# Optimization experiments

Measured on AMD Instinct MI355X. Metric: run time of the kernel, lower is better.

Reference implementation:

```python
import jax, jax.numpy as jnp
import numpy as np

EPS = 1e-6
TTT_BASE_LR = 1.0
NUM_HEADS = 16


def _ln_fused_l2_bwd(x, l2_target, gamma, beta, eps=EPS):
    # Gradient of ||LN(x)*gamma+beta - target||^2/2 wrt x (fused LN + L2 bwd).
    mu = x.mean(axis=-1, keepdims=True)
    var = ((x - mu) ** 2).mean(axis=-1, keepdims=True)
    std = jnp.sqrt(var + eps)
    x_hat = (x - mu) / std
    grad_x_hat = (gamma * x_hat + beta - l2_target) * gamma
    z = (grad_x_hat
         - grad_x_hat.mean(axis=-1, keepdims=True)
         - x_hat * (grad_x_hat * x_hat).mean(axis=-1, keepdims=True)) / std
    return z


def _ln_fwd(x, gamma, beta, eps=EPS):
    mu = x.mean(axis=-1, keepdims=True)
    var = ((x - mu) ** 2).mean(axis=-1, keepdims=True)
    x_hat = (x - mu) / jnp.sqrt(var + eps)
    return gamma * x_hat + beta


def setup_inputs() -> dict:
    key = jax.random.key(0)
    ks = jax.random.split(key, 6)
    B, L, C, H = 2, 2048, 1024, NUM_HEADS
    D = C // H
    return {
        "hidden_states": jax.random.normal(ks[0], (B, L, C), jnp.float32),
        "Wq": jax.random.normal(ks[1], (C, C), jnp.float32) * 0.02,
        "Wk": jax.random.normal(ks[2], (C, C), jnp.float32) * 0.02,
        "Wv": jax.random.normal(ks[3], (C, C), jnp.float32) * 0.02,
        "W1": jax.random.normal(ks[4], (H, D, D), jnp.float32) * 0.02,
        "b1": jnp.zeros((H, 1, D), jnp.float32),
        "ttt_norm_weight": jnp.ones((H, D), jnp.float32),
        "ttt_norm_bias": jnp.zeros((H, D), jnp.float32),
        "lr_weight": jax.random.normal(ks[5], (H, C, 1), jnp.float32) * 0.02,
        "lr_bias": jnp.zeros((H, 1), jnp.float32),
    }


def reference(hidden_states, Wq, Wk, Wv, W1, b1,
              ttt_norm_weight, ttt_norm_bias, lr_weight, lr_bias):
    B, L, C = hidden_states.shape
    H = NUM_HEADS
    D = C // H

    def proj(W):  # nn.Linear(no bias): x @ W^T, then split heads -> [B,H,L,D]
        return (hidden_states @ W.T).reshape(B, L, H, D).transpose(0, 2, 1, 3)

    XQ, XK, XV = proj(Wq), proj(Wk), proj(Wv)

    # adaptive per-token learning rate eta: [B,H,L,1]
    ttt_lr = jnp.einsum("blc,hci->bhli", hidden_states, lr_weight)
    ttt_lr = jax.nn.sigmoid(ttt_lr + lr_bias.reshape(1, H, 1, 1))
    eta = TTT_BASE_LR * ttt_lr / D

    # inner-loop forward with initial fast weights W1,b1
    Z1 = jnp.einsum("bhld,hdf->bhlf", XK, W1) + b1[None]  # [B,H,L,D]
    recon_target = XV - XK

    gamma = ttt_norm_weight.reshape(1, H, 1, D)
    beta = ttt_norm_bias.reshape(1, H, 1, D)
    grad_l_wrt_Z1 = _ln_fused_l2_bwd(Z1, recon_target, gamma, beta)

    # dual form update (batch-parallel, no state carry)
    eg = eta * grad_l_wrt_Z1                               # [B,H,L,D]
    Attn1 = jnp.einsum("bhld,bhmd->bhlm", XQ, XK)          # [B,H,L,L]
    b1_bar = b1[None] - eg.sum(axis=2, keepdims=True)      # [B,H,1,D]
    Z1_bar = (jnp.einsum("bhld,hdf->bhlf", XQ, W1)
              - jnp.einsum("bhlm,bhmd->bhld", Attn1, eg)
              + b1_bar)

    Z1_normalized = _ln_fwd(Z1_bar, gamma, beta)
    return XQ + Z1_normalized  # [B,H,L,D]
```

## Files before the change

### kernel.cpp

```cpp
#include <hip/hip_runtime.h>
#include <math.h>

#define B_ 2
#define L_ 2048
#define C_ 1024
#define H_ 16
#define D_ 64
#define BH_ (B_*H_)
#define M_ (B_*L_)
#define N_ (3*C_)
#define K_ C_
#define EPS_ 1e-6f
#define NCHUNK_ 16
#define LDT_ 136

typedef unsigned short ushort_t;
typedef short short8 __attribute__((ext_vector_type(8)));
typedef float f32x4 __attribute__((ext_vector_type(4)));
typedef unsigned short ushort4_t __attribute__((ext_vector_type(4)));

__device__ __forceinline__ ushort_t f2bf(float f) {
    union { float f; unsigned u; } v; v.f = f;
    unsigned r = v.u + 0x7FFFu + ((v.u >> 16) & 1u);
    return (ushort_t)(r >> 16);
}
__device__ __forceinline__ float bf2f(ushort_t h) {
    union { unsigned u; float f; } v; v.u = ((unsigned)h) << 16;
    return v.f;
}

__device__ __forceinline__ void gload16(const void* g, void* l) {
    __builtin_amdgcn_global_load_lds(
        (const __attribute__((address_space(1))) void*)g,
        (__attribute__((address_space(3))) void*)l, 16, 0, 0);
}

__global__ __launch_bounds__(256) void cast_eta(
    const float* __restrict__ hs, const float* __restrict__ Wq,
    const float* __restrict__ Wk, const float* __restrict__ Wv,
    const float* __restrict__ lrw, const float* __restrict__ lrb,
    ushort_t* __restrict__ hsB, ushort_t* __restrict__ Wcat,
    float* __restrict__ eta) {
    __shared__ float pA[16][257], pB[16][257];
    const int bid = blockIdx.x, t = threadIdx.x;
    if (bid < 2048) {
        const int iA = bid * 2, iB = iA + 1;
        const float* rA = hs + (size_t)iA * C_;
        const float* rB = hs + (size_t)iB * C_;
        f32x4 a = *(const f32x4*)(rA + t * 4);
        f32x4 b = *(const f32x4*)(rB + t * 4);
        ushort4_t oa, ob;
        oa.x = f2bf(a.x); oa.y = f2bf(a.y); oa.z = f2bf(a.z); oa.w = f2bf(a.w);
        ob.x = f2bf(b.x); ob.y = f2bf(b.y); ob.z = f2bf(b.z); ob.w = f2bf(b.w);
        *(ushort4_t*)(hsB + (size_t)iA * C_ + t * 4) = oa;
        *(ushort4_t*)(hsB + (size_t)iB * C_ + t * 4) = ob;
        #pragma unroll
        for (int h = 0; h < 16; ++h) {
            f32x4 w = *(const f32x4*)(lrw + (size_t)h * C_ + t * 4);
            pA[h][t] = a.x * w.x + a.y * w.y + a.z * w.z + a.w * w.w;
            pB[h][t] = b.x * w.x + b.y * w.y + b.z * w.z + b.w * w.w;
        }
        __syncthreads();
        const int h = t >> 4, seg = t & 15;
        float sA = 0.f, sB = 0.f;
        #pragma unroll
        for (int j = 0; j < 16; ++j) {
            sA += pA[h][seg * 16 + j];
            sB += pB[h][seg * 16 + j];
        }
        #pragma unroll
        for (int m = 1; m < 16; m <<= 1) {
            sA += __shfl_xor(sA, m, 64);
            sB += __shfl_xor(sB, m, 64);
        }
        if (seg == 0) {
            float bb = lrb[h];
            int bA = iA >> 11, lA = iA & (L_ - 1);
            int bB = iB >> 11, lB = iB & (L_ - 1);
            eta[((size_t)(bA * H_ + h)) * L_ + lA] =
                (1.f / (1.f + expf(-(sA + bb)))) * (1.0f / 64.0f);
            eta[((size_t)(bB * H_ + h)) * L_ + lB] =
                (1.f / (1.f + expf(-(sB + bb)))) * (1.0f / 64.0f);
        }
    } else {
        const int wb = bid - 2048;
        #pragma unroll
        for (int ii = 0; ii < 4; ++ii) {
            int cid = wb * 1024 + ii * 256 + t;
            int m = cid >> 18, r = cid & ((1 << 18) - 1);
            const float* src = (m == 0 ? Wq : (m == 1 ? Wk : Wv));
            f32x4 v = *(const f32x4*)(src + (size_t)r * 4);
            ushort4_t o;
            o.x = f2bf(v.x); o.y = f2bf(v.y); o.z = f2bf(v.z); o.w = f2bf(v.w);
            *(ushort4_t*)(Wcat + (size_t)m * (C_ * C_) + (size_t)r * 4) = o;
        }
    }
}

__global__ __launch_bounds__(256) void gemm_qkv(
    const ushort_t* __restrict__ A, const ushort_t* __restrict__ Bc,
    ushort_t* __restrict__ XQ, ushort_t* __restrict__ XK,
    ushort_t* __restrict__ XV) {
    __shared__ __align__(16) ushort_t Al[128 * 32];
    __shared__ __align__(16) ushort_t Bl[128 * 32];
    const int lid = blockIdx.x + 32 * blockIdx.y;
    const int nid = (lid & 7) * 96 + (lid >> 3);
    const int bm = nid & 31, bn = nid >> 5;
    const int t = threadIdx.x, w = t >> 6, lane = t & 63;
    const int wr = w >> 1, wc = w & 1;
    f32x4 acc[4][4];
    #pragma unroll
    for (int a = 0; a < 4; a++)
        #pragma unroll
        for (int b = 0; b < 4; b++)
            #pragma unroll
            for (int j = 0; j < 4; j++) acc[a][b][j] = 0.f;

    const int ci0 = w * 64 + lane;
    const int xread = ((lane & 15) >> 1) & 3;
    const int uslot = (lane >> 4) ^ xread;

    for (int kt = 0; kt < K_ / 32; ++kt) {
        __syncthreads();
        #pragma unroll
        for (int q = 0; q < 2; ++q) {
            int ci = q * 256 + ci0;
            int r = ci >> 2, kc = ci & 3;
            int kcp = kc ^ ((r >> 1) & 3);
            gload16(A + (size_t)(bm * 128 + r) * K_ + kt * 32 + kcp * 8,
                    &Al[q * 2048 + w * 512]);
            gload16(Bc + (size_t)(bn * 128 + r) * K_ + kt * 32 + kcp * 8,
                    &Bl[q * 2048 + w * 512]);
        }
        __syncthreads();
        short8 af[4], bfv[4];
        #pragma unroll
        for (int mf = 0; mf < 4; ++mf)
            af[mf] = *(const short8*)&Al[(wr * 64 + mf * 16 + (lane & 15)) * 32 + uslot * 8];
        #pragma unroll
        for (int nf = 0; nf < 4; ++nf)
            bfv[nf] = *(const short8*)&Bl[(wc * 64 + nf * 16 + (lane & 15)) * 32 + uslot * 8];
        #pragma unroll
        for (int mf = 0; mf < 4; ++mf)
            #pragma unroll
            for (int nf = 0; nf < 4; ++nf)
                acc[mf][nf] = __builtin_amdgcn_mfma_f32_16x16x32_bf16(
                    af[mf], bfv[nf], acc[mf][nf], 0, 0, 0);
    }

    const int jbase = bn * 128;
    const int mtx = jbase >> 10;
    ushort_t* dst = (mtx == 0) ? XQ : (mtx == 1 ? XK : XV);
    #pragma unroll
    for (int mf = 0; mf < 4; ++mf)
        #pragma unroll
        for (int nf = 0; nf < 4; ++nf)
            #pragma unroll
            for (int rg = 0; rg < 4; ++rg) {
                int i = bm * 128 + wr * 64 + mf * 16 + ((lane >> 4) << 2) + rg;
                int j = (jbase & 1023) + wc * 64 + nf * 16 + (lane & 15);
                int b = i >> 11, l = i & (L_ - 1);
                int h = j >> 6, d = j & 63;
                dst[((size_t)(b * H_ + h) * L_ + l) * D_ + d] = f2bf(acc[mf][nf][rg]);
            }
}

__global__ __launch_bounds__(256) void k2_grad2(
    const ushort_t* __restrict__ XK, const ushort_t* __restrict__ XV,
    const float* __restrict__ W1, const float* __restrict__ b1,
    const float* __restrict__ tw, const float* __restrict__ tb,
    const float* __restrict__ eta, float* __restrict__ Gp,
    float* __restrict__ bsump) {
    __shared__ __align__(16) ushort_t W1t[64 * 64];
    __shared__ __align__(16) ushort_t xkt[64 * LDT_];
    __shared__ __align__(16) ushort_t egl[64 * LDT_];
    __shared__ float b1s[64], gs[64], bes[64];
    __shared__ float sred[4][64];
    const int bh = blockIdx.y, lt = blockIdx.x;
    const int h = bh & (H_ - 1);
    const int t = threadIdx.x, w = t >> 6, lane = t & 63;
    for (int p = t; p < 4096; p += 256) {
        int e = p >> 6, f = p & 63;
        W1t[f * 64 + e] = f2bf(W1[h * 4096 + p]);
    }
    if (t < 64) { b1s[t] = b1[h * 64 + t]; gs[t] = tw[h * 64 + t]; bes[t] = tb[h * 64 + t]; }
    __syncthreads();

    const ushort_t* xk = XK + (size_t)bh * L_ * D_;
    const ushort_t* xv = XV + (size_t)bh * L_ * D_;
    const int l0 = lt * 128 + w * 32;
    const int llw = w * 32;

    f32x4 acc[2][4];
    #pragma unroll
    for (int mf = 0; mf < 2; mf++)
        #pragma unroll
        for (int nf = 0; nf < 4; nf++) {
            float bv = b1s[nf * 16 + (lane & 15)];
            #pragma unroll
            for (int j = 0; j < 4; j++) acc[mf][nf][j] = bv;
        }
    #pragma unroll
    for (int ks = 0; ks < 2; ++ks) {
        short8 af[2], bfv[4];
        const int d0 = ks * 32 + (lane >> 4) * 8;
        #pragma unroll
        for (int mf = 0; mf < 2; mf++) {
            af[mf] = *(const short8*)&xk[(size_t)(l0 + mf * 16 + (lane & 15)) * D_ + d0];
            const int ll = llw + mf * 16 + (lane & 15);
            #pragma unroll
            for (int jj = 0; jj < 8; jj++)
                xkt[(d0 + jj) * LDT_ + ll] = (ushort_t)af[mf][jj];
        }
        #pragma unroll
        for (int nf = 0; nf < 4; nf++)
            bfv[nf] = *(const short8*)&W1t[(nf * 16 + (lane & 15)) * 64 + d0];
        #pragma unroll
        for (int mf = 0; mf < 2; mf++)
            #pragma unroll
            for (int nf = 0; nf < 4; nf++)
                acc[mf][nf] = __builtin_amdgcn_mfma_f32_16x16x32_bf16(
                    af[mf], bfv[nf], acc[mf][nf], 0, 0, 0);
    }

    const float* etap = eta + (size_t)bh * L_;
    float accbs[4] = {0.f, 0.f, 0.f, 0.f};
    #pragma unroll
    for (int mf = 0; mf < 2; ++mf) {
        #pragma unroll
        for (int rg = 0; rg < 4; ++rg) {
            int lrow = l0 + mf * 16 + ((lane >> 4) << 2) + rg;
            int llr  = llw + mf * 16 + ((lane >> 4) << 2) + rg;
            float x[4], xh[4], gh[4];
            #pragma unroll
            for (int nf = 0; nf < 4; nf++) x[nf] = acc[mf][nf][rg];
            float s = x[0] + x[1] + x[2] + x[3];
            s += __shfl_xor(s, 1, 64); s += __shfl_xor(s, 2, 64);
            s += __shfl_xor(s, 4, 64); s += __shfl_xor(s, 8, 64);
            float mu = s * (1.f / 64.f);
            float vs = 0.f;
            #pragma unroll
            for (int nf = 0; nf < 4; nf++) { float dd = x[nf] - mu; vs += dd * dd; }
            vs += __shfl_xor(vs, 1, 64); vs += __shfl_xor(vs, 2, 64);
            vs += __shfl_xor(vs, 4, 64); vs += __shfl_xor(vs, 8, 64);
            float inv = 1.f / sqrtf(vs * (1.f / 64.f) + EPS_);
            float s1 = 0.f, s2 = 0.f;
            #pragma unroll
            for (int nf = 0; nf < 4; nf++) {
                int d = nf * 16 + (lane & 15);
                xh[nf] = (x[nf] - mu) * inv;
                float tgt = bf2f(xv[(size_t)lrow * D_ + d]) - bf2f(xk[(size_t)lrow * D_ + d]);
                float g = gs[d];
                gh[nf] = (g * xh[nf] + bes[d] - tgt) * g;
                s1 += gh[nf]; s2 += gh[nf] * xh[nf];
            }
            s1 += __shfl_xor(s1, 1, 64); s1 += __shfl_xor(s1, 2, 64);
            s1 += __shfl_xor(s1, 4, 64); s1 += __shfl_xor(s1, 8, 64);
            s2 += __shfl_xor(s2, 1, 64); s2 += __shfl_xor(s2, 2, 64);
            s2 += __shfl_xor(s2, 4, 64); s2 += __shfl_xor(s2, 8, 64);
            float m1 = s1 * (1.f / 64.f), m2 = s2 * (1.f / 64.f);
            float el = etap[lrow];
            #pragma unroll
            for (int nf = 0; nf < 4; nf++) {
                int d = nf * 16 + (lane & 15);
                float egv = el * ((gh[nf] - m1 - xh[nf] * m2) * inv);
                accbs[nf] += egv;
                egl[d * LDT_ + llr] = f2bf(egv);
            }
        }
    }
    #pragma unroll
    for (int nf = 0; nf < 4; nf++) {
        accbs[nf] += __shfl_xor(accbs[nf], 16, 64);
        accbs[nf] += __shfl_xor(accbs[nf], 32, 64);
    }
    if (lane < 16)
        #pragma unroll
        for (int nf = 0; nf < 4; nf++) sred[w][nf * 16 + lane] = accbs[nf];
    __syncthreads();

    f32x4 aG[4];
    #pragma unroll
    for (int nf = 0; nf < 4; nf++)
        #pragma unroll
        for (int j = 0; j < 4; j++) aG[nf][j] = 0.f;
    #pragma unroll
    for (int ks = 0; ks < 4; ++ks) {
        const int ko = ks * 32 + (lane >> 4) * 8;
        short8 ae = *(const short8*)&xkt[(w * 16 + (lane & 15)) * LDT_ + ko];
        #pragma unroll
        for (int nf = 0; nf < 4; nf++) {
            short8 be = *(const short8*)&egl[(nf * 16 + (lane & 15)) * LDT_ + ko];
            aG[nf] = __builtin_amdgcn_mfma_f32_16x16x32_bf16(ae, be, aG[nf], 0, 0, 0);
        }
    }
    float* gp = Gp + (size_t)(bh * NCHUNK_ + lt) * 4096;
    #pragma unroll
    for (int nf = 0; nf < 4; nf++)
        #pragma unroll
        for (int rg = 0; rg < 4; rg++) {
            int e = w * 16 + ((lane >> 4) << 2) + rg;
            int d = nf * 16 + (lane & 15);
            gp[e * 64 + d] = aG[nf][rg];
        }
    if (t < 64)
        bsump[(bh * NCHUNK_ + lt) * 64 + t] =
            sred[0][t] + sred[1][t] + sred[2][t] + sred[3][t];
}

__global__ __launch_bounds__(256) void k3_out(
    const ushort_t* __restrict__ XQ, const float* __restrict__ W1,
    const float* __restrict__ Gp, const float* __restrict__ b1,
    const float* __restrict__ bsump, const float* __restrict__ tw,
    const float* __restrict__ tb, float* __restrict__ out) {
    __shared__ __align__(16) ushort_t Wt[64 * 64];
    __shared__ float b1s[64], gs[64], bes[64];
    const int bh = blockIdx.y, lt = blockIdx.x;
    const int h = bh & (H_ - 1);
    const int t = threadIdx.x, w = t >> 6, lane = t & 63;
    for (int p = t; p < 4096; p += 256) {
        int e = p >> 6, f = p & 63;
        float s = W1[h * 4096 + p];
        #pragma unroll
        for (int c = 0; c < NCHUNK_; c++)
            s -= Gp[(size_t)(bh * NCHUNK_ + c) * 4096 + p];
        Wt[f * 64 + e] = f2bf(s);
    }
    if (t < 64) {
        float s = b1[h * 64 + t];
        #pragma unroll
        for (int c = 0; c < NCHUNK_; c++)
            s -= bsump[(bh * NCHUNK_ + c) * 64 + t];
        b1s[t] = s;
        gs[t] = tw[h * 64 + t]; bes[t] = tb[h * 64 + t];
    }
    __syncthreads();

    const ushort_t* xq = XQ + (size_t)bh * L_ * D_;
    const int l0 = lt * 128 + w * 32;
    f32x4 acc[2][4];
    #pragma unroll
    for (int mf = 0; mf < 2; mf++)
        #pragma unroll
        for (int nf = 0; nf < 4; nf++) {
            float bv = b1s[nf * 16 + (lane & 15)];
            #pragma unroll
            for (int j = 0; j < 4; j++) acc[mf][nf][j] = bv;
        }
    #pragma unroll
    for (int ks = 0; ks < 2; ++ks) {
        short8 af[2], bfv[4];
        #pragma unroll
        for (int mf = 0; mf < 2; mf++)
            af[mf] = *(const short8*)&xq[(size_t)(l0 + mf * 16 + (lane & 15)) * D_ + ks * 32 + (lane >> 4) * 8];
        #pragma unroll
        for (int nf = 0; nf < 4; nf++)
            bfv[nf] = *(const short8*)&Wt[(nf * 16 + (lane & 15)) * 64 + ks * 32 + (lane >> 4) * 8];
        #pragma unroll
        for (int mf = 0; mf < 2; mf++)
            #pragma unroll
            for (int nf = 0; nf < 4; nf++)
                acc[mf][nf] = __builtin_amdgcn_mfma_f32_16x16x32_bf16(
                    af[mf], bfv[nf], acc[mf][nf], 0, 0, 0);
    }

    float* outp = out + (size_t)bh * L_ * D_;
    #pragma unroll
    for (int mf = 0; mf < 2; ++mf) {
        #pragma unroll
        for (int rg = 0; rg < 4; ++rg) {
            int lrow = l0 + mf * 16 + ((lane >> 4) << 2) + rg;
            float x[4];
            #pragma unroll
            for (int nf = 0; nf < 4; nf++) x[nf] = acc[mf][nf][rg];
            float s = x[0] + x[1] + x[2] + x[3];
            s += __shfl_xor(s, 1, 64); s += __shfl_xor(s, 2, 64);
            s += __shfl_xor(s, 4, 64); s += __shfl_xor(s, 8, 64);
            float mu = s * (1.f / 64.f);
            float vs = 0.f;
            #pragma unroll
            for (int nf = 0; nf < 4; nf++) { float dd = x[nf] - mu; vs += dd * dd; }
            vs += __shfl_xor(vs, 1, 64); vs += __shfl_xor(vs, 2, 64);
            vs += __shfl_xor(vs, 4, 64); vs += __shfl_xor(vs, 8, 64);
            float inv = 1.f / sqrtf(vs * (1.f / 64.f) + EPS_);
            #pragma unroll
            for (int nf = 0; nf < 4; nf++) {
                int d = nf * 16 + (lane & 15);
                float xh = (x[nf] - mu) * inv;
                float o = gs[d] * xh + bes[d];
                float qv = bf2f(xq[(size_t)lrow * D_ + d]);
                outp[(size_t)lrow * D_ + d] = qv + o;
            }
        }
    }
}

extern "C" void kernel_launch(void* const* d_in, const int* in_sizes, int n_in,
                              void* d_out, int out_size, void* d_ws, size_t ws_size,
                              hipStream_t stream) {
    const float* hs  = (const float*)d_in[0];
    const float* Wq  = (const float*)d_in[1];
    const float* Wk  = (const float*)d_in[2];
    const float* Wv  = (const float*)d_in[3];
    const float* W1  = (const float*)d_in[4];
    const float* b1  = (const float*)d_in[5];
    const float* tw  = (const float*)d_in[6];
    const float* tb  = (const float*)d_in[7];
    const float* lrw = (const float*)d_in[8];
    const float* lrb = (const float*)d_in[9];
    float* out = (float*)d_out;

    char* ws = (char*)d_ws;
    size_t off = 0;
    ushort_t* hsB  = (ushort_t*)(ws + off); off += (size_t)M_ * K_ * 2;
    ushort_t* Wcat = (ushort_t*)(ws + off); off += (size_t)N_ * K_ * 2;
    ushort_t* XQ   = (ushort_t*)(ws + off); off += (size_t)M_ * C_ * 2;
    ushort_t* XK   = (ushort_t*)(ws + off); off += (size_t)M_ * C_ * 2;
    ushort_t* XV   = (ushort_t*)(ws + off); off += (size_t)M_ * C_ * 2;
    float*    eta  = (float*)(ws + off);    off += (size_t)BH_ * L_ * 4;
    float*    Gp    = (float*)hsB;
    float*    bsump = (float*)Wcat;

    cast_eta<<<2048 + 768, 256, 0, stream>>>(hs, Wq, Wk, Wv, lrw, lrb, hsB, Wcat, eta);
    gemm_qkv<<<dim3(M_ / 128, N_ / 128), 256, 0, stream>>>(hsB, Wcat, XQ, XK, XV);
    k2_grad2<<<dim3(L_ / 128, BH_), 256, 0, stream>>>(XK, XV, W1, b1, tw, tb, eta, Gp, bsump);
    k3_out<<<dim3(L_ / 128, BH_), 256, 0, stream>>>(XQ, W1, Gp, b1, bsump, tw, tb, out);
}
```

Measured before the change: 81.93 us.

## Rewrite QKV GEMM with 256x256 tiles and double-buffered LDS prefetch

The QKV projection GEMM is restructured around 256x256 output tiles with 512 threads, a K-step of 64 and two LDS buffers. The next K tile's global-to-LDS loads are interleaved between MFMA phases, with barriers and s_setprio around the compute bursts, so load latency overlaps with matrix math. An XOR swizzle keeps LDS reads conflict-free. The trade-off is the grid: it shrinks to 192 blocks, fewer than the CUs, and the old XCD-aware block remapping is dropped, so some hardware may sit idle. The larger LDS footprint also likely allows only one block per CU.

New measurement: 82.87 us. About the same (+1.1%).

```diff
diff --git a/kernel.cpp b/kernel.cpp
--- a/kernel.cpp
+++ b/kernel.cpp
@@ -97,70 +97,123 @@
     }
 }
 
-__global__ __launch_bounds__(256) void gemm_qkv(
+__global__ __launch_bounds__(512, 2) void gemm_qkv(
     const ushort_t* __restrict__ A, const ushort_t* __restrict__ Bc,
     ushort_t* __restrict__ XQ, ushort_t* __restrict__ XK,
     ushort_t* __restrict__ XV) {
-    __shared__ __align__(16) ushort_t Al[128 * 32];
-    __shared__ __align__(16) ushort_t Bl[128 * 32];
-    const int lid = blockIdx.x + 32 * blockIdx.y;
-    const int nid = (lid & 7) * 96 + (lid >> 3);
-    const int bm = nid & 31, bn = nid >> 5;
-    const int t = threadIdx.x, w = t >> 6, lane = t & 63;
-    const int wr = w >> 1, wc = w & 1;
-    f32x4 acc[4][4];
-    #pragma unroll
-    for (int a = 0; a < 4; a++)
-        #pragma unroll
-        for (int b = 0; b < 4; b++)
-            #pragma unroll
-            for (int j = 0; j < 4; j++) acc[a][b][j] = 0.f;
-
-    const int ci0 = w * 64 + lane;
-    const int xread = ((lane & 15) >> 1) & 3;
-    const int uslot = (lane >> 4) ^ xread;
-
-    for (int kt = 0; kt < K_ / 32; ++kt) {
-        __syncthreads();
-        #pragma unroll
-        for (int q = 0; q < 2; ++q) {
-            int ci = q * 256 + ci0;
-            int r = ci >> 2, kc = ci & 3;
-            int kcp = kc ^ ((r >> 1) & 3);
-            gload16(A + (size_t)(bm * 128 + r) * K_ + kt * 32 + kcp * 8,
-                    &Al[q * 2048 + w * 512]);
-            gload16(Bc + (size_t)(bn * 128 + r) * K_ + kt * 32 + kcp * 8,
-                    &Bl[q * 2048 + w * 512]);
-        }
-        __syncthreads();
-        short8 af[4], bfv[4];
-        #pragma unroll
-        for (int mf = 0; mf < 4; ++mf)
-            af[mf] = *(const short8*)&Al[(wr * 64 + mf * 16 + (lane & 15)) * 32 + uslot * 8];
+    __shared__ __align__(16) ushort_t Al[2][256 * 64];
+    __shared__ __align__(16) ushort_t Bl[2][256 * 64];
+    const int bm = blockIdx.x, bn = blockIdx.y;
+    const int t = threadIdx.x, lane = t & 63, w = t >> 6;
+    const int wm = w >> 2, wn = w & 3;
+    f32x4 acc[8][4];
+    #pragma unroll
+    for (int mf = 0; mf < 8; ++mf)
         #pragma unroll
         for (int nf = 0; nf < 4; ++nf)
-            bfv[nf] = *(const short8*)&Bl[(wc * 64 + nf * 16 + (lane & 15)) * 32 + uslot * 8];
+            #pragma unroll
+            for (int j = 0; j < 4; ++j) acc[mf][nf][j] = 0.f;
+
+#define STAGE_PASS(bi, kt, p) do {                                          \
+        int li_ = (p) * 512 + t; int r_ = li_ >> 3;                         \
+        int us_ = (li_ & 7) ^ (r_ & 7);                                     \
+        gload16(A + (size_t)(bm * 256 + r_) * K_ + (kt) * 64 + us_ * 8,     \
+                &Al[bi][li_ * 8]);                                          \
+        gload16(Bc + (size_t)(bn * 256 + r_) * K_ + (kt) * 64 + us_ * 8,    \
+                &Bl[bi][li_ * 8]);                                          \
+    } while (0)
+
+    const int la15 = lane & 15, la4 = lane >> 4;
+#define RD_A(bi, mf, ks) (*(const short8*)&Al[bi][                          \
+        (wm * 128 + (mf) * 16 + la15) * 64 +                                \
+        ((((ks) * 4 + la4) ^ ((wm * 128 + (mf) * 16 + la15) & 7)) * 8)])
+#define RD_B(bi, nf, ks) (*(const short8*)&Bl[bi][                          \
+        (wn * 64 + (nf) * 16 + la15) * 64 +                                 \
+        ((((ks) * 4 + la4) ^ ((wn * 64 + (nf) * 16 + la15) & 7)) * 8)])
+
+    STAGE_PASS(0, 0, 0); STAGE_PASS(0, 0, 1);
+    STAGE_PASS(0, 0, 2); STAGE_PASS(0, 0, 3);
+    asm volatile("s_waitcnt vmcnt(0)" ::: "memory");
+    __builtin_amdgcn_s_barrier();
+
+    for (int kt = 0; kt < 16; ++kt) {
+        const int c = kt & 1;
+        const bool pf = (kt < 15);
+        short8 bf0[4], bf1[4], afr[4];
+        #pragma unroll
+        for (int nf = 0; nf < 4; ++nf) bf0[nf] = RD_B(c, nf, 0);
+        #pragma unroll
+        for (int mf = 0; mf < 4; ++mf) afr[mf] = RD_A(c, mf, 0);
+        if (pf) { STAGE_PASS(c ^ 1, kt + 1, 0); STAGE_PASS(c ^ 1, kt + 1, 1); }
+        __builtin_amdgcn_s_barrier();
+        __builtin_amdgcn_s_setprio(1);
         #pragma unroll
         for (int mf = 0; mf < 4; ++mf)
             #pragma unroll
             for (int nf = 0; nf < 4; ++nf)
                 acc[mf][nf] = __builtin_amdgcn_mfma_f32_16x16x32_bf16(
-                    af[mf], bfv[nf], acc[mf][nf], 0, 0, 0);
-    }
-
-    const int jbase = bn * 128;
-    const int mtx = jbase >> 10;
+                    afr[mf], bf0[nf], acc[mf][nf], 0, 0, 0);
+        __builtin_amdgcn_s_setprio(0);
+        __builtin_amdgcn_s_barrier();
+        #pragma unroll
+        for (int nf = 0; nf < 4; ++nf) bf1[nf] = RD_B(c, nf, 1);
+        #pragma unroll
+        for (int mf = 0; mf < 4; ++mf) afr[mf] = RD_A(c, mf, 1);
+        if (pf) STAGE_PASS(c ^ 1, kt + 1, 2);
+        __builtin_amdgcn_s_barrier();
+        __builtin_amdgcn_s_setprio(1);
+        #pragma unroll
+        for (int mf = 0; mf < 4; ++mf)
+            #pragma unroll
+            for (int nf = 0; nf < 4; ++nf)
+                acc[mf][nf] = __builtin_amdgcn_mfma_f32_16x16x32_bf16(
+                    afr[mf], bf1[nf], acc[mf][nf], 0, 0, 0);
+        __builtin_amdgcn_s_setprio(0);
+        __builtin_amdgcn_s_barrier();
+        #pragma unroll
+        for (int mf = 0; mf < 4; ++mf) afr[mf] = RD_A(c, mf + 4, 0);
+        if (pf) STAGE_PASS(c ^ 1, kt + 1, 3);
+        __builtin_amdgcn_s_barrier();
+        __builtin_amdgcn_s_setprio(1);
+        #pragma unroll
+        for (int mf = 0; mf < 4; ++mf)
+            #pragma unroll
+            for (int nf = 0; nf < 4; ++nf)
+                acc[mf + 4][nf] = __builtin_amdgcn_mfma_f32_16x16x32_bf16(
+                    afr[mf], bf0[nf], acc[mf + 4][nf], 0, 0, 0);
+        __builtin_amdgcn_s_setprio(0);
+        __builtin_amdgcn_s_barrier();
+        #pragma unroll
+        for (int mf = 0; mf < 4; ++mf) afr[mf] = RD_A(c, mf + 4, 1);
+        __builtin_amdgcn_s_barrier();
+        __builtin_amdgcn_s_setprio(1);
+        #pragma unroll
+        for (int mf = 0; mf < 4; ++mf)
+            #pragma unroll
+            for (int nf = 0; nf < 4; ++nf)
+                acc[mf + 4][nf] = __builtin_amdgcn_mfma_f32_16x16x32_bf16(
+                    afr[mf], bf1[nf], acc[mf + 4][nf], 0, 0, 0);
+        __builtin_amdgcn_s_setprio(0);
+        asm volatile("s_waitcnt vmcnt(0)" ::: "memory");
+        __builtin_amdgcn_s_barrier();
+    }
+#undef STAGE_PASS
+#undef RD_A
+#undef RD_B
+
+    const int mtx = bn >> 2;
     ushort_t* dst = (mtx == 0) ? XQ : (mtx == 1 ? XK : XV);
-    #pragma unroll
-    for (int mf = 0; mf < 4; ++mf)
+    const int jb = (bn & 3) * 256 + wn * 64;
+    #pragma unroll
+    for (int mf = 0; mf < 8; ++mf)
         #pragma unroll
         for (int nf = 0; nf < 4; ++nf)
             #pragma unroll
             for (int rg = 0; rg < 4; ++rg) {
-                int i = bm * 128 + wr * 64 + mf * 16 + ((lane >> 4) << 2) + rg;
-                int j = (jbase & 1023) + wc * 64 + nf * 16 + (lane & 15);
+                int i = bm * 256 + wm * 128 + mf * 16 + la4 * 4 + rg;
+                int jj = jb + nf * 16 + la15;
                 int b = i >> 11, l = i & (L_ - 1);
-                int h = j >> 6, d = j & 63;
+                int h = jj >> 6, d = jj & 63;
                 dst[((size_t)(b * H_ + h) * L_ + l) * D_ + d] = f2bf(acc[mf][nf][rg]);
             }
 }
@@ -422,7 +475,7 @@
     float*    bsump = (float*)Wcat;
 
     cast_eta<<<2048 + 768, 256, 0, stream>>>(hs, Wq, Wk, Wv, lrw, lrb, hsB, Wcat, eta);
-    gemm_qkv<<<dim3(M_ / 128, N_ / 128), 256, 0, stream>>>(hsB, Wcat, XQ, XK, XV);
+    gemm_qkv<<<dim3(M_ / 256, N_ / 256), 512, 0, stream>>>(hsB, Wcat, XQ, XK, XV);
     k2_grad2<<<dim3(L_ / 128, BH_), 256, 0, stream>>>(XK, XV, W1, b1, tw, tb, eta, Gp, bsump);
     k3_out<<<dim3(L_ / 128, BH_), 256, 0, stream>>>(XQ, W1, Gp, b1, bsump, tw, tb, out);
 }
```

## Fold Wv-Wk into weights, stage GEMM epilogue via LDS, drop tile swizzle

Applied to the files above, without the earlier changes.

The weight-cast step now builds the third projection matrix as Wv-Wk, so the GEMM writes the reconstruction target directly and the gradient kernel reads one bf16 tensor instead of two. The GEMM epilogue now stages the accumulator tile in shared memory and writes 16-byte vectors per row, replacing scattered 2-byte stores into the head-major layout. The block-index remapping that grouped tiles for L2 reuse is removed and plain blockIdx order is used. Subtracting the weights in fp32 before rounding to bf16 slightly changes numerics, and the epilogue adds extra barriers and a larger shared-memory footprint.

Result: no change. 80.62 us (-1.6%).

```diff
diff --git a/kernel.cpp b/kernel.cpp
--- a/kernel.cpp
+++ b/kernel.cpp
@@ -88,8 +88,15 @@
         for (int ii = 0; ii < 4; ++ii) {
             int cid = wb * 1024 + ii * 256 + t;
             int m = cid >> 18, r = cid & ((1 << 18) - 1);
-            const float* src = (m == 0 ? Wq : (m == 1 ? Wk : Wv));
-            f32x4 v = *(const f32x4*)(src + (size_t)r * 4);
+            f32x4 v;
+            if (m == 0)      v = *(const f32x4*)(Wq + (size_t)r * 4);
+            else if (m == 1) v = *(const f32x4*)(Wk + (size_t)r * 4);
+            else {
+                f32x4 vv = *(const f32x4*)(Wv + (size_t)r * 4);
+                f32x4 vk = *(const f32x4*)(Wk + (size_t)r * 4);
+                v.x = vv.x - vk.x; v.y = vv.y - vk.y;
+                v.z = vv.z - vk.z; v.w = vv.w - vk.w;
+            }
             ushort4_t o;
             o.x = f2bf(v.x); o.y = f2bf(v.y); o.z = f2bf(v.z); o.w = f2bf(v.w);
             *(ushort4_t*)(Wcat + (size_t)m * (C_ * C_) + (size_t)r * 4) = o;
@@ -100,14 +107,14 @@
 __global__ __launch_bounds__(256) void gemm_qkv(
     const ushort_t* __restrict__ A, const ushort_t* __restrict__ Bc,
     ushort_t* __restrict__ XQ, ushort_t* __restrict__ XK,
-    ushort_t* __restrict__ XV) {
-    __shared__ __align__(16) ushort_t Al[128 * 32];
-    __shared__ __align__(16) ushort_t Bl[128 * 32];
-    const int lid = blockIdx.x + 32 * blockIdx.y;
-    const int nid = (lid & 7) * 96 + (lid >> 3);
-    const int bm = nid & 31, bn = nid >> 5;
+    ushort_t* __restrict__ XT) {
+    __shared__ __align__(16) ushort_t smem[128 * 136];
+    ushort_t* Al = smem;
+    ushort_t* Bl = smem + 4096;
+    const int bm = blockIdx.x, bn = blockIdx.y;
     const int t = threadIdx.x, w = t >> 6, lane = t & 63;
     const int wr = w >> 1, wc = w & 1;
+    const int la15 = lane & 15, la4 = lane >> 4;
     f32x4 acc[4][4];
     #pragma unroll
     for (int a = 0; a < 4; a++)
@@ -117,8 +124,8 @@
             for (int j = 0; j < 4; j++) acc[a][b][j] = 0.f;
 
     const int ci0 = w * 64 + lane;
-    const int xread = ((lane & 15) >> 1) & 3;
-    const int uslot = (lane >> 4) ^ xread;
+    const int xread = (la15 >> 1) & 3;
+    const int uslot = la4 ^ xread;
 
     for (int kt = 0; kt < K_ / 32; ++kt) {
         __syncthreads();
@@ -136,10 +143,10 @@
         short8 af[4], bfv[4];
         #pragma unroll
         for (int mf = 0; mf < 4; ++mf)
-            af[mf] = *(const short8*)&Al[(wr * 64 + mf * 16 + (lane & 15)) * 32 + uslot * 8];
+            af[mf] = *(const short8*)&Al[(wr * 64 + mf * 16 + la15) * 32 + uslot * 8];
         #pragma unroll
         for (int nf = 0; nf < 4; ++nf)
-            bfv[nf] = *(const short8*)&Bl[(wc * 64 + nf * 16 + (lane & 15)) * 32 + uslot * 8];
+            bfv[nf] = *(const short8*)&Bl[(wc * 64 + nf * 16 + la15) * 32 + uslot * 8];
         #pragma unroll
         for (int mf = 0; mf < 4; ++mf)
             #pragma unroll
@@ -148,25 +155,36 @@
                     af[mf], bfv[nf], acc[mf][nf], 0, 0, 0);
     }
 
+    __syncthreads();
+    #pragma unroll
+    for (int mf = 0; mf < 4; ++mf)
+        #pragma unroll
+        for (int nf = 0; nf < 4; ++nf)
+            #pragma unroll
+            for (int rg = 0; rg < 4; ++rg) {
+                int i = wr * 64 + mf * 16 + la4 * 4 + rg;
+                int j = wc * 64 + nf * 16 + la15;
+                smem[i * 136 + j] = f2bf(acc[mf][nf][rg]);
+            }
+    __syncthreads();
     const int jbase = bn * 128;
     const int mtx = jbase >> 10;
-    ushort_t* dst = (mtx == 0) ? XQ : (mtx == 1 ? XK : XV);
-    #pragma unroll
-    for (int mf = 0; mf < 4; ++mf)
-        #pragma unroll
-        for (int nf = 0; nf < 4; ++nf)
-            #pragma unroll
-            for (int rg = 0; rg < 4; ++rg) {
-                int i = bm * 128 + wr * 64 + mf * 16 + ((lane >> 4) << 2) + rg;
-                int j = (jbase & 1023) + wc * 64 + nf * 16 + (lane & 15);
-                int b = i >> 11, l = i & (L_ - 1);
-                int h = j >> 6, d = j & 63;
-                dst[((size_t)(b * H_ + h) * L_ + l) * D_ + d] = f2bf(acc[mf][nf][rg]);
-            }
+    ushort_t* dst = (mtx == 0) ? XQ : (mtx == 1 ? XK : XT);
+    const int hb = (jbase & 1023) >> 6;
+    #pragma unroll
+    for (int pass = 0; pass < 8; ++pass) {
+        int i = pass * 16 + (t >> 4);
+        int jj = (t & 15) * 8;
+        short8 v = *(const short8*)&smem[i * 136 + jj];
+        int ig = bm * 128 + i;
+        int b = ig >> 11, l = ig & (L_ - 1);
+        int h = hb + (jj >> 6), d = jj & 63;
+        *(short8*)&dst[((size_t)(b * H_ + h) * L_ + l) * D_ + d] = v;
+    }
 }
 
 __global__ __launch_bounds__(256) void k2_grad2(
-    const ushort_t* __restrict__ XK, const ushort_t* __restrict__ XV,
+    const ushort_t* __restrict__ XK, const ushort_t* __restrict__ XT,
     const float* __restrict__ W1, const float* __restrict__ b1,
     const float* __restrict__ tw, const float* __restrict__ tb,
     const float* __restrict__ eta, float* __restrict__ Gp,
@@ -187,7 +205,7 @@
     __syncthreads();
 
     const ushort_t* xk = XK + (size_t)bh * L_ * D_;
-    const ushort_t* xv = XV + (size_t)bh * L_ * D_;
+    const ushort_t* xt = XT + (size_t)bh * L_ * D_;
     const int l0 = lt * 128 + w * 32;
     const int llw = w * 32;
 
@@ -249,7 +267,7 @@
             for (int nf = 0; nf < 4; nf++) {
                 int d = nf * 16 + (lane & 15);
                 xh[nf] = (x[nf] - mu) * inv;
-                float tgt = bf2f(xv[(size_t)lrow * D_ + d]) - bf2f(xk[(size_t)lrow * D_ + d]);
+                float tgt = bf2f(xt[(size_t)lrow * D_ + d]);
                 float g = gs[d];
                 gh[nf] = (g * xh[nf] + bes[d] - tgt) * g;
                 s1 += gh[nf]; s2 += gh[nf] * xh[nf];
@@ -416,13 +434,13 @@
     ushort_t* Wcat = (ushort_t*)(ws + off); off += (size_t)N_ * K_ * 2;
     ushort_t* XQ   = (ushort_t*)(ws + off); off += (size_t)M_ * C_ * 2;
     ushort_t* XK   = (ushort_t*)(ws + off); off += (size_t)M_ * C_ * 2;
-    ushort_t* XV   = (ushort_t*)(ws + off); off += (size_t)M_ * C_ * 2;
+    ushort_t* XT   = (ushort_t*)(ws + off); off += (size_t)M_ * C_ * 2;
     float*    eta  = (float*)(ws + off);    off += (size_t)BH_ * L_ * 4;
     float*    Gp    = (float*)hsB;
     float*    bsump = (float*)Wcat;
 
     cast_eta<<<2048 + 768, 256, 0, stream>>>(hs, Wq, Wk, Wv, lrw, lrb, hsB, Wcat, eta);
-    gemm_qkv<<<dim3(M_ / 128, N_ / 128), 256, 0, stream>>>(hsB, Wcat, XQ, XK, XV);
-    k2_grad2<<<dim3(L_ / 128, BH_), 256, 0, stream>>>(XK, XV, W1, b1, tw, tb, eta, Gp, bsump);
+    gemm_qkv<<<dim3(M_ / 128, N_ / 128), 256, 0, stream>>>(hsB, Wcat, XQ, XK, XT);
+    k2_grad2<<<dim3(L_ / 128, BH_), 256, 0, stream>>>(XK, XT, W1, b1, tw, tb, eta, Gp, bsump);
     k3_out<<<dim3(L_ / 128, BH_), 256, 0, stream>>>(XQ, W1, Gp, b1, bsump, tw, tb, out);
 }
```
